# Performance work log

Measured on AMD Instinct MI355X. Metric: run time of the kernel, lower is better.

Reference implementation:

```python
import jax, jax.numpy as jnp
import numpy as np
import math

N_EMBD = 1024
N_HEAD = 16
B, T = 2, 2048
MASK_VAL = -10.0  # non-standard soft mask value from original module


def setup_inputs() -> dict:
    key = jax.random.key(0)
    k1, k2, k3 = jax.random.split(key, 3)
    scale = 1.0 / math.sqrt(N_EMBD)
    x = jax.random.normal(k1, (B, T, N_EMBD), dtype=jnp.float32)
    # torch Linear weights: (out_features, in_features)
    w_attn = jax.random.normal(k2, (3 * N_EMBD, N_EMBD), dtype=jnp.float32) * scale
    w_proj = jax.random.normal(k3, (N_EMBD, N_EMBD), dtype=jnp.float32) * scale
    return {"x": x, "w_attn": w_attn, "w_proj": w_proj}


def reference(x, w_attn, w_proj):
    Bsz, Tlen, C = x.shape
    hs = C // N_HEAD
    qkv = jnp.einsum('btc,fc->btf', x, w_attn)  # [B,T,3C]
    q, k, v = jnp.split(qkv, 3, axis=-1)
    # [B,H,T,hs]
    q = q.reshape(Bsz, Tlen, N_HEAD, hs).transpose(0, 2, 1, 3)
    k = k.reshape(Bsz, Tlen, N_HEAD, hs).transpose(0, 2, 1, 3)
    v = v.reshape(Bsz, Tlen, N_HEAD, hs).transpose(0, 2, 1, 3)
    att = jnp.einsum('bhqd,bhkd->bhqk', q, k) * (1.0 / math.sqrt(hs))
    causal = jnp.tril(jnp.ones((Tlen, Tlen), dtype=bool))
    att = jnp.where(causal[None, None], att, MASK_VAL)
    att = jax.nn.softmax(att, axis=-1)
    y = jnp.einsum('bhqk,bhkd->bhqd', att, v)
    y = y.transpose(0, 2, 1, 3).reshape(Bsz, Tlen, C)
    return jnp.einsum('btc,fc->btf', y, w_proj)
```

## Files before the change

### kernel.cpp

```cpp
#include <hip/hip_runtime.h>
#include <hip/hip_bf16.h>
#include <stdint.h>

#define BSZ   2
#define TT    2048
#define NH    16
#define HS    64
#define CC    1024
#define C3    3072
#define MT    4096
#define E10   4.5399929762484854e-05f
#define SCL2  0.1803368801111204f

typedef __bf16 bf16;
typedef __bf16 bf16x8 __attribute__((ext_vector_type(8)));
typedef float  f32x4  __attribute__((ext_vector_type(4)));
typedef short  s16x4  __attribute__((ext_vector_type(4)));

#define AS1 __attribute__((address_space(1)))
#define AS3 __attribute__((address_space(3)))

__device__ __forceinline__ void glds16(const bf16* g, bf16* l) {
    __builtin_amdgcn_global_load_lds((const AS1 void*)g, (AS3 void*)l, 16, 0, 0);
}

__global__ void detect_dtype(const uint16_t* __restrict__ x, int* __restrict__ flag) {
    __shared__ int cnt;
    if (threadIdx.x == 0) cnt = 0;
    __syncthreads();
    int local = 0;
    for (int i = threadIdx.x; i < 512; i += 256) {
        uint16_t u = x[i];
        int e = (u >> 7) & 0xFF;
        if (e >= 96 && e <= 159) local++;
    }
    atomicAdd(&cnt, local);
    __syncthreads();
    if (threadIdx.x == 0) *flag = (cnt >= 461) ? 0 : 1;
}

#define NX8  (MT * CC / 8)
#define NWA8 (C3 * CC / 8)
#define NWP8 (CC * CC / 8)
__global__ __launch_bounds__(256)
void convert_all(const float* __restrict__ x, const float* __restrict__ wa,
                 const float* __restrict__ wp, bf16* __restrict__ xd,
                 bf16* __restrict__ wad, bf16* __restrict__ wpd,
                 const int* __restrict__ flag) {
    if (*flag == 0) return;
    long i = (long)blockIdx.x * 256 + threadIdx.x;
    const float* s; bf16* d; long off;
    if (i < NX8)             { s = x;  d = xd;  off = i; }
    else if (i < NX8 + NWA8) { s = wa; d = wad; off = i - NX8; }
    else                     { s = wp; d = wpd; off = i - NX8 - NWA8; }
    const float4* sp = reinterpret_cast<const float4*>(s) + off * 2;
    float4 a = sp[0], b = sp[1];
    bf16x8 r;
    r[0] = (bf16)a.x; r[1] = (bf16)a.y; r[2] = (bf16)a.z; r[3] = (bf16)a.w;
    r[4] = (bf16)b.x; r[5] = (bf16)b.y; r[6] = (bf16)b.z; r[7] = (bf16)b.w;
    reinterpret_cast<bf16x8*>(d)[off] = r;
}

__global__ __launch_bounds__(256)
void gemm_bt(const bf16* __restrict__ A0, const bf16* __restrict__ A1,
             const bf16* __restrict__ B0, const bf16* __restrict__ B1,
             void* __restrict__ Cmain, bf16* __restrict__ Cv,
             const int* __restrict__ flag,
             int M, int N, int K, int lda, int ldb, int ldc,
             int split_col, int cf32_dyn) {
    __shared__ bf16 As[2][128 * 32];
    __shared__ bf16 Bs[2][128 * 32];

    const int f = *flag;
    const bf16* A = f ? A1 : A0;
    const bf16* B = f ? B1 : B0;
    const int cf32 = cf32_dyn & f;

    const int tid  = threadIdx.x;
    const int lane = tid & 63;
    const int wave = tid >> 6;
    const int wm   = wave >> 1;
    const int wn   = wave & 1;
    const int quad = lane >> 4;
    const int l16  = lane & 15;

    const int row0 = blockIdx.y * 128;
    const int col0 = blockIdx.x * 128;

    const int srow = tid >> 2;
    const int skk  = (tid & 3) * 8;

    const bf16* Ap = A + (long)(row0 + srow) * lda + skk;
    const bf16* Bp = B + (long)(col0 + srow) * ldb + skk;

    auto stage = [&](int k0, int buf) {
        glds16(Ap + k0,                  &As[buf][wave * 512]);
        glds16(Ap + (long)64 * lda + k0, &As[buf][wave * 512 + 2048]);
        glds16(Bp + k0,                  &Bs[buf][wave * 512]);
        glds16(Bp + (long)64 * ldb + k0, &Bs[buf][wave * 512 + 2048]);
    };

    f32x4 acc[4][4] = {};
    stage(0, 0);

    for (int k0 = 0; k0 < K; k0 += 32) {
        const int buf = (k0 >> 5) & 1;
        __syncthreads();
        if (k0 + 32 < K) stage(k0 + 32, buf ^ 1);

        const bf16* Ac = As[buf];
        const bf16* Bc = Bs[buf];
        bf16x8 af[4], bfv[4];
#pragma unroll
        for (int mi = 0; mi < 4; ++mi)
            af[mi] = *reinterpret_cast<const bf16x8*>(&Ac[(wm * 64 + mi * 16 + l16) * 32 + quad * 8]);
#pragma unroll
        for (int ni = 0; ni < 4; ++ni)
            bfv[ni] = *reinterpret_cast<const bf16x8*>(&Bc[(wn * 64 + ni * 16 + l16) * 32 + quad * 8]);
#pragma unroll
        for (int mi = 0; mi < 4; ++mi)
#pragma unroll
            for (int ni = 0; ni < 4; ++ni)
                acc[mi][ni] = __builtin_amdgcn_mfma_f32_16x16x32_bf16(af[mi], bfv[ni], acc[mi][ni], 0, 0, 0);
    }

    if (split_col < 0 || col0 < split_col) {
#pragma unroll
        for (int mi = 0; mi < 4; ++mi)
#pragma unroll
            for (int ni = 0; ni < 4; ++ni)
#pragma unroll
                for (int r = 0; r < 4; ++r) {
                    int row = row0 + wm * 64 + mi * 16 + quad * 4 + r;
                    int col = col0 + wn * 64 + ni * 16 + l16;
                    float v = acc[mi][ni][r];
                    if (cf32) ((float*)Cmain)[(long)row * ldc + col] = v;
                    else      ((bf16*)Cmain)[(long)row * ldc + col] = (bf16)v;
                }
    } else {
        const int h  = (col0 - split_col + wn * 64) >> 6;
        const int bq = row0 >> 11;
        const int tc = ((row0 & 2047) >> 6) + wm;
#pragma unroll
        for (int ni = 0; ni < 4; ++ni) {
            long vrow = (long)(bq * NH + h) * 64 + ni * 16 + l16;
#pragma unroll
            for (int mi = 0; mi < 4; ++mi) {
                bf16 outv[4];
#pragma unroll
                for (int r = 0; r < 4; ++r) outv[r] = (bf16)acc[mi][ni][r];
                *reinterpret_cast<uint2*>(&Cv[vrow * 2048 + tc * 64 + quad * 16 + mi * 4]) =
                    *reinterpret_cast<uint2*>(outv);
            }
        }
    }
}

__global__ __launch_bounds__(256)
void gemm_bt64(const bf16* __restrict__ A0, const bf16* __restrict__ A1,
               const bf16* __restrict__ B0, const bf16* __restrict__ B1,
               void* __restrict__ C, const int* __restrict__ flag,
               int M, int N, int K, int lda, int ldb, int ldc, int cf32_dyn) {
    __shared__ bf16 As[2][128 * 32];
    __shared__ bf16 Bs[2][64 * 32];

    const int f = *flag;
    const bf16* A = f ? A1 : A0;
    const bf16* B = f ? B1 : B0;
    const int cf32 = cf32_dyn & f;

    const int tid  = threadIdx.x;
    const int lane = tid & 63;
    const int wave = tid >> 6;
    const int wm   = wave >> 1;
    const int wn   = wave & 1;
    const int quad = lane >> 4;
    const int l16  = lane & 15;

    const int row0 = blockIdx.y * 128;
    const int col0 = blockIdx.x * 64;

    const int srow = tid >> 2;
    const int skk  = (tid & 3) * 8;

    const bf16* Ap = A + (long)(row0 + srow) * lda + skk;
    const bf16* Bp = B + (long)(col0 + srow) * ldb + skk;

    auto stage = [&](int k0, int buf) {
        glds16(Ap + k0,                  &As[buf][wave * 512]);
        glds16(Ap + (long)64 * lda + k0, &As[buf][wave * 512 + 2048]);
        glds16(Bp + k0,                  &Bs[buf][wave * 512]);
    };

    f32x4 acc[4][2] = {};
    stage(0, 0);

    for (int k0 = 0; k0 < K; k0 += 32) {
        const int buf = (k0 >> 5) & 1;
        __syncthreads();
        if (k0 + 32 < K) stage(k0 + 32, buf ^ 1);

        const bf16* Ac = As[buf];
        const bf16* Bc = Bs[buf];
        bf16x8 af[4], bfv[2];
#pragma unroll
        for (int mi = 0; mi < 4; ++mi)
            af[mi] = *reinterpret_cast<const bf16x8*>(&Ac[(wm * 64 + mi * 16 + l16) * 32 + quad * 8]);
#pragma unroll
        for (int ni = 0; ni < 2; ++ni)
            bfv[ni] = *reinterpret_cast<const bf16x8*>(&Bc[(wn * 32 + ni * 16 + l16) * 32 + quad * 8]);
#pragma unroll
        for (int mi = 0; mi < 4; ++mi)
#pragma unroll
            for (int ni = 0; ni < 2; ++ni)
                acc[mi][ni] = __builtin_amdgcn_mfma_f32_16x16x32_bf16(af[mi], bfv[ni], acc[mi][ni], 0, 0, 0);
    }

#pragma unroll
    for (int mi = 0; mi < 4; ++mi)
#pragma unroll
        for (int ni = 0; ni < 2; ++ni)
#pragma unroll
            for (int r = 0; r < 4; ++r) {
                int row = row0 + wm * 64 + mi * 16 + quad * 4 + r;
                int col = col0 + wn * 32 + ni * 16 + l16;
                float v = acc[mi][ni][r];
                if (cf32) ((float*)C)[(long)row * ldc + col] = v;
                else      ((bf16*)C)[(long)row * ldc + col] = (bf16)v;
            }
}

__global__ __launch_bounds__(256)
void vtile2(const bf16* __restrict__ Vt, float* __restrict__ Vtile) {
    const int kt = blockIdx.x, bh = blockIdx.y;
    const int tid = threadIdx.x;
    const int d = tid >> 2, part = tid & 3;
    const bf16* p = Vt + ((long)bh * 64 + d) * 2048 + kt * 64 + part * 16;
    float s = 0.f;
#pragma unroll
    for (int i = 0; i < 2; ++i) {
        bf16x8 v = *reinterpret_cast<const bf16x8*>(p + i * 8);
#pragma unroll
        for (int j = 0; j < 8; ++j) s += (float)v[j];
    }
    s += __shfl_xor(s, 1, 64);
    s += __shfl_xor(s, 2, 64);
    if (part == 0) Vtile[((long)bh * 32 + kt) * 64 + d] = s;
}

__global__ void vts_suffix(const float* __restrict__ Vtile, float* __restrict__ Vts) {
    const int bh = blockIdx.x, d = threadIdx.x;
    Vts[((long)bh * 33 + 32) * 64 + d] = 0.f;
    float acc = 0.f;
    for (int kt = 31; kt >= 0; --kt) {
        acc += Vtile[((long)bh * 32 + kt) * 64 + d];
        Vts[((long)bh * 33 + kt) * 64 + d] = acc;
    }
}

__global__ __launch_bounds__(256)
void attn(bf16* __restrict__ qk, const bf16* __restrict__ Vt,
          const float* __restrict__ Vts) {
    __shared__ bf16 Ks[2][64 * 64];
    __shared__ bf16 Vs[2][64 * 64];

    const int tid  = threadIdx.x;
    const int lane = tid & 63;
    const int wave = tid >> 6;
    const int quad = lane >> 4;
    const int l16  = lane & 15;

    const int f2   = blockIdx.x;
    const int xcd  = f2 & 7;
    const int slot = f2 >> 3;
    const int bh   = (slot & 3) * 8 + xcd;
    const int chunk = 31 - (slot >> 2);
    const int b = bh >> 4, h = bh & 15;
    const int q0 = chunk * 64;
    const long rbase = (long)b * TT;

    const bf16* qp = qk + (rbase + q0 + wave * 16 + l16) * 2048 + h * HS;
    bf16x8 qf0 = *reinterpret_cast<const bf16x8*>(qp + quad * 8);
    bf16x8 qf1 = *reinterpret_cast<const bf16x8*>(qp + 32 + quad * 8);

    f32x4 O[4] = {};
    float lp = 0.f;

    const int rl  = lane >> 3;
    const int cs  = (lane & 7) ^ rl;
    const int row0dma = wave * 16 + rl;
    const bf16* kgb = qk + (rbase + row0dma) * 2048 + CC + h * HS + cs * 8;
    const bf16* vgb = Vt + ((long)(b * NH + h) * 64 + row0dma) * 2048 + cs * 8;
    const int sx = l16 & 7;

    auto stage = [&](int kt, int buf) {
        glds16(kgb + (long)(kt * 64) * 2048,     &Ks[buf][wave * 1024]);
        glds16(kgb + (long)(kt * 64 + 8) * 2048, &Ks[buf][wave * 1024 + 512]);
        glds16(vgb + kt * 64,                    &Vs[buf][wave * 1024]);
        glds16(vgb + 8 * 2048 + kt * 64,         &Vs[buf][wave * 1024 + 512]);
    };

    const int ktend = chunk + 1;
    stage(0, 0);

    for (int kt = 0; kt < ktend; ++kt) {
        const int buf = kt & 1;
        __syncthreads();
        if (kt + 1 < ktend) stage(kt + 1, buf ^ 1);

        const bf16* Kc = Ks[buf];
        const bf16* Vc = Vs[buf];

        bf16x8 kf0[4], kf1[4];
#pragma unroll
        for (int g = 0; g < 4; ++g) {
            const int krow = g * 16 + l16;
            kf0[g] = *reinterpret_cast<const bf16x8*>(&Kc[krow * 64 + ((quad ^ sx) * 8)]);
            kf1[g] = *reinterpret_cast<const bf16x8*>(&Kc[krow * 64 + (((4 + quad) ^ sx) * 8)]);
        }
        s16x4 vf[4][4];
#pragma unroll
        for (int dg = 0; dg < 4; ++dg) {
            const int vrow = dg * 16 + l16;
            union { uint4 u; s16x4 s[2]; } ua, ub;
            ua.u = *reinterpret_cast<const uint4*>(&Vc[vrow * 64 + (((2 * quad) ^ sx) * 8)]);
            ub.u = *reinterpret_cast<const uint4*>(&Vc[vrow * 64 + (((2 * quad + 1) ^ sx) * 8)]);
            vf[dg][0] = ua.s[0]; vf[dg][1] = ua.s[1];
            vf[dg][2] = ub.s[0]; vf[dg][3] = ub.s[1];
        }

        f32x4 S[4] = {};
#pragma unroll
        for (int g = 0; g < 4; ++g) {
            S[g] = __builtin_amdgcn_mfma_f32_16x16x32_bf16(kf0[g], qf0, S[g], 0, 0, 0);
            S[g] = __builtin_amdgcn_mfma_f32_16x16x32_bf16(kf1[g], qf1, S[g], 0, 0, 0);
        }

        const bool dtile = (kt == chunk);
        const int ql = wave * 16 + l16;
        s16x4 pk[4];
#pragma unroll
        for (int g = 0; g < 4; ++g) {
#pragma unroll
            for (int r = 0; r < 4; ++r) {
                float p = __builtin_exp2f(S[g][r] * SCL2);
                if (dtile) {
                    int kl = g * 16 + quad * 4 + r;
                    p = (kl > ql) ? E10 : p;
                }
                lp += p;
                union { bf16 b_; short s_; } u;
                u.b_ = (bf16)p;
                pk[g][r] = u.s_;
            }
        }

#pragma unroll
        for (int dg = 0; dg < 4; ++dg) {
            O[dg] = __builtin_amdgcn_mfma_f32_16x16x16bf16_1k(vf[dg][0], pk[0], O[dg], 0, 0, 0);
            O[dg] = __builtin_amdgcn_mfma_f32_16x16x16bf16_1k(vf[dg][1], pk[1], O[dg], 0, 0, 0);
            O[dg] = __builtin_amdgcn_mfma_f32_16x16x16bf16_1k(vf[dg][2], pk[2], O[dg], 0, 0, 0);
            O[dg] = __builtin_amdgcn_mfma_f32_16x16x16bf16_1k(vf[dg][3], pk[3], O[dg], 0, 0, 0);
        }
    }

    lp += __shfl_xor(lp, 16, 64);
    lp += __shfl_xor(lp, 32, 64);

    const int nfut = TT - ktend * 64;
    const float l = lp + (float)nfut * E10;
    const float invl = 1.0f / l;
    const float* vfp = Vts + ((long)(b * NH + h) * 33 + ktend) * 64;

    bf16* yp = qk + (rbase + q0 + wave * 16 + l16) * 2048 + h * HS;
#pragma unroll
    for (int dg = 0; dg < 4; ++dg) {
        bf16 outv[4];
#pragma unroll
        for (int r = 0; r < 4; ++r) {
            float o = O[dg][r] + E10 * vfp[dg * 16 + quad * 4 + r];
            outv[r] = (bf16)(o * invl);
        }
        *reinterpret_cast<uint2*>(yp + dg * 16 + quad * 4) =
            *reinterpret_cast<uint2*>(outv);
    }
}

extern "C" void kernel_launch(void* const* d_in, const int* in_sizes, int n_in,
                              void* d_out, int out_size, void* d_ws, size_t ws_size,
                              hipStream_t stream) {
    const void* x      = d_in[0];
    const void* w_attn = d_in[1];
    const void* w_proj = d_in[2];

    char* ws = (char*)d_ws;
    bf16*  qk     = (bf16*)ws;
    bf16*  Vt     = (bf16*)(ws + (size_t)MT * 2048 * 2);
    char*  p2     = ws + (size_t)MT * 2048 * 2 + (size_t)32 * 64 * 2048 * 2;
    int*   flag   = (int*)p2;
    float* Vts    = (float*)(p2 + 256);
    bf16*  wp_cvt = (bf16*)(p2 + 256 + 32 * 33 * 64 * 4);
    float* Vtile  = (float*)((char*)wp_cvt + (size_t)CC * CC * 2);

    bf16* x_cvt  = (bf16*)d_out;
    bf16* wa_cvt = (bf16*)d_out + (size_t)MT * CC;

    detect_dtype<<<1, 256, 0, stream>>>((const uint16_t*)x, flag);
    convert_all<<<(NX8 + NWA8 + NWP8) / 256, 256, 0, stream>>>(
        (const float*)x, (const float*)w_attn, (const float*)w_proj,
        x_cvt, wa_cvt, wp_cvt, flag);

    gemm_bt<<<dim3(C3 / 128, MT / 128), 256, 0, stream>>>(
        (const bf16*)x, x_cvt, (const bf16*)w_attn, wa_cvt, qk, Vt, flag,
        MT, C3, CC, CC, CC, 2048, 2048, 0);

    vtile2<<<dim3(32, BSZ * NH), 256, 0, stream>>>(Vt, Vtile);
    vts_suffix<<<dim3(BSZ * NH), dim3(64), 0, stream>>>(Vtile, Vts);

    attn<<<dim3(1024), 256, 0, stream>>>(qk, Vt, Vts);

    gemm_bt64<<<dim3(CC / 64, MT / 128), 256, 0, stream>>>(
        qk, qk, (const bf16*)w_proj, wp_cvt, d_out, flag,
        MT, CC, CC, 2048, CC, CC, 1);
}
```

Baseline: 182.0 us.

## Process two query sub-tiles per attention block to reuse K/V tiles

Each attention block now covers 128 query rows as two 64-row sub-tiles that share every staged K/V tile, which halves the grid and roughly halves K/V global-to-LDS traffic per query. Chunk ordering is reworked to pair long and short causal chunks so the load stays balanced, and s_setprio is placed around the MFMA groups. The cost is higher register pressure from the doubled O accumulators (launch bounds now ask for 2 blocks per CU) and fewer blocks available to fill the machine.

Result: slower. 198.4 us (+9.0%).

```diff
diff --git a/kernel.cpp b/kernel.cpp
--- a/kernel.cpp
+++ b/kernel.cpp
@@ -258,7 +258,7 @@
     }
 }
 
-__global__ __launch_bounds__(256)
+__global__ __launch_bounds__(256, 2)
 void attn(bf16* __restrict__ qk, const bf16* __restrict__ Vt,
           const float* __restrict__ Vts) {
     __shared__ bf16 Ks[2][64 * 64];
@@ -274,17 +274,23 @@
     const int xcd  = f2 & 7;
     const int slot = f2 >> 3;
     const int bh   = (slot & 3) * 8 + xcd;
-    const int chunk = 31 - (slot >> 2);
+    const int g    = slot >> 2;
+    const int chunk = (g < 8) ? (15 - g) : (g - 8);
     const int b = bh >> 4, h = bh & 15;
-    const int q0 = chunk * 64;
+    const int q0 = chunk * 128;
     const long rbase = (long)b * TT;
-
-    const bf16* qp = qk + (rbase + q0 + wave * 16 + l16) * 2048 + h * HS;
-    bf16x8 qf0 = *reinterpret_cast<const bf16x8*>(qp + quad * 8);
-    bf16x8 qf1 = *reinterpret_cast<const bf16x8*>(qp + 32 + quad * 8);
-
-    f32x4 O[4] = {};
-    float lp = 0.f;
+    const int ktend = 2 * chunk + 2;
+
+    bf16x8 qf[2][2];
+#pragma unroll
+    for (int s = 0; s < 2; ++s) {
+        const bf16* qp = qk + (rbase + q0 + s * 64 + wave * 16 + l16) * 2048 + h * HS;
+        qf[s][0] = *reinterpret_cast<const bf16x8*>(qp + quad * 8);
+        qf[s][1] = *reinterpret_cast<const bf16x8*>(qp + 32 + quad * 8);
+    }
+
+    f32x4 O[2][4] = {};
+    float lp[2] = {0.f, 0.f};
 
     const int rl  = lane >> 3;
     const int cs  = (lane & 7) ^ rl;
@@ -300,7 +306,6 @@
         glds16(vgb + 8 * 2048 + kt * 64,         &Vs[buf][wave * 1024 + 512]);
     };
 
-    const int ktend = chunk + 1;
     stage(0, 0);
 
     for (int kt = 0; kt < ktend; ++kt) {
@@ -313,10 +318,10 @@
 
         bf16x8 kf0[4], kf1[4];
 #pragma unroll
-        for (int g = 0; g < 4; ++g) {
-            const int krow = g * 16 + l16;
-            kf0[g] = *reinterpret_cast<const bf16x8*>(&Kc[krow * 64 + ((quad ^ sx) * 8)]);
-            kf1[g] = *reinterpret_cast<const bf16x8*>(&Kc[krow * 64 + (((4 + quad) ^ sx) * 8)]);
+        for (int gg = 0; gg < 4; ++gg) {
+            const int krow = gg * 16 + l16;
+            kf0[gg] = *reinterpret_cast<const bf16x8*>(&Kc[krow * 64 + ((quad ^ sx) * 8)]);
+            kf1[gg] = *reinterpret_cast<const bf16x8*>(&Kc[krow * 64 + (((4 + quad) ^ sx) * 8)]);
         }
         s16x4 vf[4][4];
 #pragma unroll
@@ -329,60 +334,74 @@
             vf[dg][2] = ub.s[0]; vf[dg][3] = ub.s[1];
         }
 
-        f32x4 S[4] = {};
-#pragma unroll
-        for (int g = 0; g < 4; ++g) {
-            S[g] = __builtin_amdgcn_mfma_f32_16x16x32_bf16(kf0[g], qf0, S[g], 0, 0, 0);
-            S[g] = __builtin_amdgcn_mfma_f32_16x16x32_bf16(kf1[g], qf1, S[g], 0, 0, 0);
+#pragma unroll
+        for (int s = 0; s < 2; ++s) {
+            if (s == 0 && kt == ktend - 1) continue;
+
+            f32x4 S[4] = {};
+            __builtin_amdgcn_s_setprio(1);
+#pragma unroll
+            for (int gg = 0; gg < 4; ++gg) {
+                S[gg] = __builtin_amdgcn_mfma_f32_16x16x32_bf16(kf0[gg], qf[s][0], S[gg], 0, 0, 0);
+                S[gg] = __builtin_amdgcn_mfma_f32_16x16x32_bf16(kf1[gg], qf[s][1], S[gg], 0, 0, 0);
+            }
+            __builtin_amdgcn_s_setprio(0);
+
+            const bool dtile = (kt == ktend - 2 + s);
+            const int ql = wave * 16 + l16;
+            s16x4 pk[4];
+#pragma unroll
+            for (int gg = 0; gg < 4; ++gg) {
+#pragma unroll
+                for (int r = 0; r < 4; ++r) {
+                    float p = __builtin_exp2f(S[gg][r] * SCL2);
+                    if (dtile) {
+                        int kl = gg * 16 + quad * 4 + r;
+                        p = (kl > ql) ? E10 : p;
+                    }
+                    lp[s] += p;
+                    union { bf16 b_; short s_; } u;
+                    u.b_ = (bf16)p;
+                    pk[gg][r] = u.s_;
+                }
+            }
+
+            __builtin_amdgcn_s_setprio(1);
+#pragma unroll
+            for (int dg = 0; dg < 4; ++dg) {
+                O[s][dg] = __builtin_amdgcn_mfma_f32_16x16x16bf16_1k(vf[dg][0], pk[0], O[s][dg], 0, 0, 0);
+                O[s][dg] = __builtin_amdgcn_mfma_f32_16x16x16bf16_1k(vf[dg][1], pk[1], O[s][dg], 0, 0, 0);
+                O[s][dg] = __builtin_amdgcn_mfma_f32_16x16x16bf16_1k(vf[dg][2], pk[2], O[s][dg], 0, 0, 0);
+                O[s][dg] = __builtin_amdgcn_mfma_f32_16x16x16bf16_1k(vf[dg][3], pk[3], O[s][dg], 0, 0, 0);
+            }
+            __builtin_amdgcn_s_setprio(0);
         }
-
-        const bool dtile = (kt == chunk);
-        const int ql = wave * 16 + l16;
-        s16x4 pk[4];
-#pragma unroll
-        for (int g = 0; g < 4; ++g) {
+    }
+
+#pragma unroll
+    for (int s = 0; s < 2; ++s) {
+        float lps = lp[s];
+        lps += __shfl_xor(lps, 16, 64);
+        lps += __shfl_xor(lps, 32, 64);
+
+        const int kte = ktend - 1 + s;
+        const int nfut = TT - kte * 64;
+        const float l = lps + (float)nfut * E10;
+        const float invl = 1.0f / l;
+        const float* vfp = Vts + ((long)(b * NH + h) * 33 + kte) * 64;
+
+        bf16* yp = qk + (rbase + q0 + s * 64 + wave * 16 + l16) * 2048 + h * HS;
+#pragma unroll
+        for (int dg = 0; dg < 4; ++dg) {
+            bf16 outv[4];
 #pragma unroll
             for (int r = 0; r < 4; ++r) {
-                float p = __builtin_exp2f(S[g][r] * SCL2);
-                if (dtile) {
-                    int kl = g * 16 + quad * 4 + r;
-                    p = (kl > ql) ? E10 : p;
-                }
-                lp += p;
-                union { bf16 b_; short s_; } u;
-                u.b_ = (bf16)p;
-                pk[g][r] = u.s_;
-            }
+                float o = O[s][dg][r] + E10 * vfp[dg * 16 + quad * 4 + r];
+                outv[r] = (bf16)(o * invl);
+            }
+            *reinterpret_cast<uint2*>(yp + dg * 16 + quad * 4) =
+                *reinterpret_cast<uint2*>(outv);
         }
-
-#pragma unroll
-        for (int dg = 0; dg < 4; ++dg) {
-            O[dg] = __builtin_amdgcn_mfma_f32_16x16x16bf16_1k(vf[dg][0], pk[0], O[dg], 0, 0, 0);
-            O[dg] = __builtin_amdgcn_mfma_f32_16x16x16bf16_1k(vf[dg][1], pk[1], O[dg], 0, 0, 0);
-            O[dg] = __builtin_amdgcn_mfma_f32_16x16x16bf16_1k(vf[dg][2], pk[2], O[dg], 0, 0, 0);
-            O[dg] = __builtin_amdgcn_mfma_f32_16x16x16bf16_1k(vf[dg][3], pk[3], O[dg], 0, 0, 0);
-        }
-    }
-
-    lp += __shfl_xor(lp, 16, 64);
-    lp += __shfl_xor(lp, 32, 64);
-
-    const int nfut = TT - ktend * 64;
-    const float l = lp + (float)nfut * E10;
-    const float invl = 1.0f / l;
-    const float* vfp = Vts + ((long)(b * NH + h) * 33 + ktend) * 64;
-
-    bf16* yp = qk + (rbase + q0 + wave * 16 + l16) * 2048 + h * HS;
-#pragma unroll
-    for (int dg = 0; dg < 4; ++dg) {
-        bf16 outv[4];
-#pragma unroll
-        for (int r = 0; r < 4; ++r) {
-            float o = O[dg][r] + E10 * vfp[dg * 16 + quad * 4 + r];
-            outv[r] = (bf16)(o * invl);
-        }
-        *reinterpret_cast<uint2*>(yp + dg * 16 + quad * 4) =
-            *reinterpret_cast<uint2*>(outv);
     }
 }
 
@@ -417,7 +436,7 @@
     vtile2<<<dim3(32, BSZ * NH), 256, 0, stream>>>(Vt, Vtile);
     vts_suffix<<<dim3(BSZ * NH), dim3(64), 0, stream>>>(Vtile, Vts);
 
-    attn<<<dim3(1024), 256, 0, stream>>>(qk, Vt, Vts);
+    attn<<<dim3(512), 256, 0, stream>>>(qk, Vt, Vts);
 
     gemm_bt64<<<dim3(CC / 64, MT / 128), 256, 0, stream>>>(
         qk, qk, (const bf16*)w_proj, wp_cvt, d_out, flag,
```

## Shrink attention tiles to 32 rows with 2-wave blocks for finer causal work

Applied to the files above, without the earlier changes.

The attention kernel now processes 32-query chunks with 32-key tiles using 128-thread blocks (2048 blocks), and the V-tile prefix sums are computed at 32-key granularity. The GEMM's transposed-V store layout is permuted so the 16x16x16 MFMA fragment reads match the narrower 32-column V tiles. The aim is to cut wasted work on the causal diagonal, balance the triangular workload better, and raise occupancy. In exchange, K/V tiles are reused across fewer queries and there are more loop iterations and barriers per unit of work.

New measurement: 196.7 us. 8.1% more time.

```diff
diff --git a/kernel.cpp b/kernel.cpp
--- a/kernel.cpp
+++ b/kernel.cpp
@@ -149,7 +149,8 @@
                 bf16 outv[4];
 #pragma unroll
                 for (int r = 0; r < 4; ++r) outv[r] = (bf16)acc[mi][ni][r];
-                *reinterpret_cast<uint2*>(&Cv[vrow * 2048 + tc * 64 + quad * 16 + mi * 4]) =
+                *reinterpret_cast<uint2*>(
+                    &Cv[vrow * 2048 + tc * 64 + (mi >> 1) * 32 + quad * 8 + (mi & 1) * 4]) =
                     *reinterpret_cast<uint2*>(outv);
             }
         }
@@ -244,25 +245,25 @@
         for (int j = 0; j < 8; ++j) s += (float)v[j];
     }
     s += __shfl_xor(s, 1, 64);
-    s += __shfl_xor(s, 2, 64);
-    if (part == 0) Vtile[((long)bh * 32 + kt) * 64 + d] = s;
+    if ((part & 1) == 0)
+        Vtile[((long)bh * 64 + kt * 2 + (part >> 1)) * 64 + d] = s;
 }
 
 __global__ void vts_suffix(const float* __restrict__ Vtile, float* __restrict__ Vts) {
     const int bh = blockIdx.x, d = threadIdx.x;
-    Vts[((long)bh * 33 + 32) * 64 + d] = 0.f;
+    Vts[((long)bh * 65 + 64) * 64 + d] = 0.f;
     float acc = 0.f;
-    for (int kt = 31; kt >= 0; --kt) {
-        acc += Vtile[((long)bh * 32 + kt) * 64 + d];
-        Vts[((long)bh * 33 + kt) * 64 + d] = acc;
-    }
-}
-
-__global__ __launch_bounds__(256)
+    for (int kt = 63; kt >= 0; --kt) {
+        acc += Vtile[((long)bh * 64 + kt) * 64 + d];
+        Vts[((long)bh * 65 + kt) * 64 + d] = acc;
+    }
+}
+
+__global__ __launch_bounds__(128, 4)
 void attn(bf16* __restrict__ qk, const bf16* __restrict__ Vt,
           const float* __restrict__ Vts) {
-    __shared__ bf16 Ks[2][64 * 64];
-    __shared__ bf16 Vs[2][64 * 64];
+    __shared__ bf16 Ks[2][32 * 64];
+    __shared__ bf16 Vs[2][64 * 32];
 
     const int tid  = threadIdx.x;
     const int lane = tid & 63;
@@ -274,10 +275,11 @@
     const int xcd  = f2 & 7;
     const int slot = f2 >> 3;
     const int bh   = (slot & 3) * 8 + xcd;
-    const int chunk = 31 - (slot >> 2);
+    const int chunk = 63 - (slot >> 2);
     const int b = bh >> 4, h = bh & 15;
-    const int q0 = chunk * 64;
+    const int q0 = chunk * 32;
     const long rbase = (long)b * TT;
+    const int ktend = chunk + 1;
 
     const bf16* qp = qk + (rbase + q0 + wave * 16 + l16) * 2048 + h * HS;
     bf16x8 qf0 = *reinterpret_cast<const bf16x8*>(qp + quad * 8);
@@ -288,19 +290,21 @@
 
     const int rl  = lane >> 3;
     const int cs  = (lane & 7) ^ rl;
-    const int row0dma = wave * 16 + rl;
-    const bf16* kgb = qk + (rbase + row0dma) * 2048 + CC + h * HS + cs * 8;
-    const bf16* vgb = Vt + ((long)(b * NH + h) * 64 + row0dma) * 2048 + cs * 8;
+    const bf16* kgb = qk + (rbase + wave * 16 + rl) * 2048 + CC + h * HS + cs * 8;
+    const int rlv = lane >> 2;
+    const int csv = (lane & 3) ^ (rlv & 3);
+    const bf16* vgb = Vt + ((long)(b * NH + h) * 64 + wave * 32 + rlv) * 2048 + csv * 8;
+
     const int sx = l16 & 7;
+    const int sv = l16 & 3;
 
     auto stage = [&](int kt, int buf) {
-        glds16(kgb + (long)(kt * 64) * 2048,     &Ks[buf][wave * 1024]);
-        glds16(kgb + (long)(kt * 64 + 8) * 2048, &Ks[buf][wave * 1024 + 512]);
-        glds16(vgb + kt * 64,                    &Vs[buf][wave * 1024]);
-        glds16(vgb + 8 * 2048 + kt * 64,         &Vs[buf][wave * 1024 + 512]);
+        glds16(kgb + (long)(kt * 32) * 2048,     &Ks[buf][wave * 1024]);
+        glds16(kgb + (long)(kt * 32 + 8) * 2048, &Ks[buf][wave * 1024 + 512]);
+        glds16(vgb + kt * 32,                    &Vs[buf][wave * 1024]);
+        glds16(vgb + (long)16 * 2048 + kt * 32,  &Vs[buf][wave * 1024 + 512]);
     };
 
-    const int ktend = chunk + 1;
     stage(0, 0);
 
     for (int kt = 0; kt < ktend; ++kt) {
@@ -311,47 +315,45 @@
         const bf16* Kc = Ks[buf];
         const bf16* Vc = Vs[buf];
 
-        bf16x8 kf0[4], kf1[4];
-#pragma unroll
-        for (int g = 0; g < 4; ++g) {
-            const int krow = g * 16 + l16;
-            kf0[g] = *reinterpret_cast<const bf16x8*>(&Kc[krow * 64 + ((quad ^ sx) * 8)]);
-            kf1[g] = *reinterpret_cast<const bf16x8*>(&Kc[krow * 64 + (((4 + quad) ^ sx) * 8)]);
-        }
-        s16x4 vf[4][4];
+        bf16x8 kf0[2], kf1[2];
+#pragma unroll
+        for (int gg = 0; gg < 2; ++gg) {
+            const int krow = gg * 16 + l16;
+            kf0[gg] = *reinterpret_cast<const bf16x8*>(&Kc[krow * 64 + ((quad ^ sx) * 8)]);
+            kf1[gg] = *reinterpret_cast<const bf16x8*>(&Kc[krow * 64 + (((4 + quad) ^ sx) * 8)]);
+        }
+        s16x4 vf[4][2];
 #pragma unroll
         for (int dg = 0; dg < 4; ++dg) {
             const int vrow = dg * 16 + l16;
-            union { uint4 u; s16x4 s[2]; } ua, ub;
-            ua.u = *reinterpret_cast<const uint4*>(&Vc[vrow * 64 + (((2 * quad) ^ sx) * 8)]);
-            ub.u = *reinterpret_cast<const uint4*>(&Vc[vrow * 64 + (((2 * quad + 1) ^ sx) * 8)]);
+            union { uint4 u; s16x4 s[2]; } ua;
+            ua.u = *reinterpret_cast<const uint4*>(&Vc[vrow * 32 + ((quad ^ sv) * 8)]);
             vf[dg][0] = ua.s[0]; vf[dg][1] = ua.s[1];
-            vf[dg][2] = ub.s[0]; vf[dg][3] = ub.s[1];
-        }
-
-        f32x4 S[4] = {};
-#pragma unroll
-        for (int g = 0; g < 4; ++g) {
-            S[g] = __builtin_amdgcn_mfma_f32_16x16x32_bf16(kf0[g], qf0, S[g], 0, 0, 0);
-            S[g] = __builtin_amdgcn_mfma_f32_16x16x32_bf16(kf1[g], qf1, S[g], 0, 0, 0);
-        }
-
-        const bool dtile = (kt == chunk);
+        }
+
+        f32x4 S[2] = {};
+#pragma unroll
+        for (int gg = 0; gg < 2; ++gg) {
+            S[gg] = __builtin_amdgcn_mfma_f32_16x16x32_bf16(kf0[gg], qf0, S[gg], 0, 0, 0);
+            S[gg] = __builtin_amdgcn_mfma_f32_16x16x32_bf16(kf1[gg], qf1, S[gg], 0, 0, 0);
+        }
+
+        const bool dtile = (kt == ktend - 1);
         const int ql = wave * 16 + l16;
-        s16x4 pk[4];
-#pragma unroll
-        for (int g = 0; g < 4; ++g) {
+        s16x4 pk[2];
+#pragma unroll
+        for (int gg = 0; gg < 2; ++gg) {
 #pragma unroll
             for (int r = 0; r < 4; ++r) {
-                float p = __builtin_exp2f(S[g][r] * SCL2);
+                float p = __builtin_exp2f(S[gg][r] * SCL2);
                 if (dtile) {
-                    int kl = g * 16 + quad * 4 + r;
+                    int kl = gg * 16 + quad * 4 + r;
                     p = (kl > ql) ? E10 : p;
                 }
                 lp += p;
                 union { bf16 b_; short s_; } u;
                 u.b_ = (bf16)p;
-                pk[g][r] = u.s_;
+                pk[gg][r] = u.s_;
             }
         }
 
@@ -359,18 +361,16 @@
         for (int dg = 0; dg < 4; ++dg) {
             O[dg] = __builtin_amdgcn_mfma_f32_16x16x16bf16_1k(vf[dg][0], pk[0], O[dg], 0, 0, 0);
             O[dg] = __builtin_amdgcn_mfma_f32_16x16x16bf16_1k(vf[dg][1], pk[1], O[dg], 0, 0, 0);
-            O[dg] = __builtin_amdgcn_mfma_f32_16x16x16bf16_1k(vf[dg][2], pk[2], O[dg], 0, 0, 0);
-            O[dg] = __builtin_amdgcn_mfma_f32_16x16x16bf16_1k(vf[dg][3], pk[3], O[dg], 0, 0, 0);
         }
     }
 
     lp += __shfl_xor(lp, 16, 64);
     lp += __shfl_xor(lp, 32, 64);
 
-    const int nfut = TT - ktend * 64;
+    const int nfut = TT - ktend * 32;
     const float l = lp + (float)nfut * E10;
     const float invl = 1.0f / l;
-    const float* vfp = Vts + ((long)(b * NH + h) * 33 + ktend) * 64;
+    const float* vfp = Vts + ((long)bh * 65 + ktend) * 64;
 
     bf16* yp = qk + (rbase + q0 + wave * 16 + l16) * 2048 + h * HS;
 #pragma unroll
@@ -399,7 +399,7 @@
     char*  p2     = ws + (size_t)MT * 2048 * 2 + (size_t)32 * 64 * 2048 * 2;
     int*   flag   = (int*)p2;
     float* Vts    = (float*)(p2 + 256);
-    bf16*  wp_cvt = (bf16*)(p2 + 256 + 32 * 33 * 64 * 4);
+    bf16*  wp_cvt = (bf16*)(p2 + 256 + 32 * 65 * 64 * 4);
     float* Vtile  = (float*)((char*)wp_cvt + (size_t)CC * CC * 2);
 
     bf16* x_cvt  = (bf16*)d_out;
@@ -417,7 +417,7 @@
     vtile2<<<dim3(32, BSZ * NH), 256, 0, stream>>>(Vt, Vtile);
     vts_suffix<<<dim3(BSZ * NH), dim3(64), 0, stream>>>(Vtile, Vts);
 
-    attn<<<dim3(1024), 256, 0, stream>>>(qk, Vt, Vts);
+    attn<<<dim3(2048), 128, 0, stream>>>(qk, Vt, Vts);
 
     gemm_bt64<<<dim3(CC / 64, MT / 128), 256, 0, stream>>>(
         qk, qk, (const bf16*)w_proj, wp_cvt, d_out, flag,
```

## Triple-buffer K/V tiles with vmcnt waits, MFMA priority, and head-pair XCD mapping

Applied to the files above, without the earlier changes.

Moves the attention kernel's K/V shared-memory staging from double to triple buffering. Each iteration now waits on a partial vmcnt instead of draining all loads, so two tiles stay in flight. It also raises wave priority around the MFMA blocks and remaps block indices so each XCD handles adjacent head pairs for both batches, which may improve L2 locality. The extra LDS (48KB per block) and the launch-bound hint of 3 could limit occupancy, and the hand-counted vmcnt(4) depends on each stage issuing exactly four loads.

Measured after the change: 185.7 us. 1.02x slower.

```diff
diff --git a/kernel.cpp b/kernel.cpp
--- a/kernel.cpp
+++ b/kernel.cpp
@@ -258,11 +258,11 @@
     }
 }
 
-__global__ __launch_bounds__(256)
+__global__ __launch_bounds__(256, 3)
 void attn(bf16* __restrict__ qk, const bf16* __restrict__ Vt,
           const float* __restrict__ Vts) {
-    __shared__ bf16 Ks[2][64 * 64];
-    __shared__ bf16 Vs[2][64 * 64];
+    __shared__ bf16 Ks[3][64 * 64];
+    __shared__ bf16 Vs[3][64 * 64];
 
     const int tid  = threadIdx.x;
     const int lane = tid & 63;
@@ -273,11 +273,14 @@
     const int f2   = blockIdx.x;
     const int xcd  = f2 & 7;
     const int slot = f2 >> 3;
-    const int bh   = (slot & 3) * 8 + xcd;
+    const int u    = slot & 3;
     const int chunk = 31 - (slot >> 2);
-    const int b = bh >> 4, h = bh & 15;
+    const int h = xcd * 2 + (u & 1);
+    const int b = u >> 1;
+    const int bh = b * 16 + h;
     const int q0 = chunk * 64;
     const long rbase = (long)b * TT;
+    const int ktend = chunk + 1;
 
     const bf16* qp = qk + (rbase + q0 + wave * 16 + l16) * 2048 + h * HS;
     bf16x8 qf0 = *reinterpret_cast<const bf16x8*>(qp + quad * 8);
@@ -300,16 +303,21 @@
         glds16(vgb + 8 * 2048 + kt * 64,         &Vs[buf][wave * 1024 + 512]);
     };
 
-    const int ktend = chunk + 1;
     stage(0, 0);
-
+    stage(ktend > 1 ? 1 : 0, 1);
+
+    int rb = 0;
+    int sb = 2;
     for (int kt = 0; kt < ktend; ++kt) {
-        const int buf = kt & 1;
-        __syncthreads();
-        if (kt + 1 < ktend) stage(kt + 1, buf ^ 1);
-
-        const bf16* Kc = Ks[buf];
-        const bf16* Vc = Vs[buf];
+        asm volatile("s_waitcnt vmcnt(4)" ::: "memory");
+        __builtin_amdgcn_s_barrier();
+        __builtin_amdgcn_sched_barrier(0);
+
+        int nkt = kt + 2; nkt = (nkt < ktend) ? nkt : (ktend - 1);
+        stage(nkt, sb);
+
+        const bf16* Kc = Ks[rb];
+        const bf16* Vc = Vs[rb];
 
         bf16x8 kf0[4], kf1[4];
 #pragma unroll
@@ -330,13 +338,15 @@
         }
 
         f32x4 S[4] = {};
+        __builtin_amdgcn_s_setprio(1);
 #pragma unroll
         for (int g = 0; g < 4; ++g) {
             S[g] = __builtin_amdgcn_mfma_f32_16x16x32_bf16(kf0[g], qf0, S[g], 0, 0, 0);
             S[g] = __builtin_amdgcn_mfma_f32_16x16x32_bf16(kf1[g], qf1, S[g], 0, 0, 0);
         }
-
-        const bool dtile = (kt == chunk);
+        __builtin_amdgcn_s_setprio(0);
+
+        const bool dtile = (kt == ktend - 1);
         const int ql = wave * 16 + l16;
         s16x4 pk[4];
 #pragma unroll
@@ -349,12 +359,13 @@
                     p = (kl > ql) ? E10 : p;
                 }
                 lp += p;
-                union { bf16 b_; short s_; } u;
-                u.b_ = (bf16)p;
-                pk[g][r] = u.s_;
+                union { bf16 b_; short s_; } u2;
+                u2.b_ = (bf16)p;
+                pk[g][r] = u2.s_;
             }
         }
 
+        __builtin_amdgcn_s_setprio(1);
 #pragma unroll
         for (int dg = 0; dg < 4; ++dg) {
             O[dg] = __builtin_amdgcn_mfma_f32_16x16x16bf16_1k(vf[dg][0], pk[0], O[dg], 0, 0, 0);
@@ -362,6 +373,10 @@
             O[dg] = __builtin_amdgcn_mfma_f32_16x16x16bf16_1k(vf[dg][2], pk[2], O[dg], 0, 0, 0);
             O[dg] = __builtin_amdgcn_mfma_f32_16x16x16bf16_1k(vf[dg][3], pk[3], O[dg], 0, 0, 0);
         }
+        __builtin_amdgcn_s_setprio(0);
+
+        rb = (rb == 2) ? 0 : rb + 1;
+        sb = (sb == 2) ? 0 : sb + 1;
     }
 
     lp += __shfl_xor(lp, 16, 64);
@@ -370,7 +385,7 @@
     const int nfut = TT - ktend * 64;
     const float l = lp + (float)nfut * E10;
     const float invl = 1.0f / l;
-    const float* vfp = Vts + ((long)(b * NH + h) * 33 + ktend) * 64;
+    const float* vfp = Vts + ((long)bh * 33 + ktend) * 64;
 
     bf16* yp = qk + (rbase + q0 + wave * 16 + l16) * 2048 + h * HS;
 #pragma unroll
```
